# Performance work log

Hardware: AMD Instinct MI355X
Metric: run time of the kernel (lower is better)

The kernel has to match this reference:

```python
import jax, jax.numpy as jnp
import numpy as np

B, CH, H, W, D = 2, 32, 256, 512, 192


def setup_inputs() -> dict:
    key = jax.random.key(0)
    ks = jax.random.split(key, 10)
    def w(k, shape, fan_in):
        return jax.random.normal(k, shape, jnp.float32) * (1.0 / np.sqrt(fan_in))
    return {
        "x": jax.random.normal(ks[0], (B, CH, H, W), jnp.float32),
        "y": jax.random.normal(ks[1], (B, CH, H, W), jnp.float32),
        # encoder: 1x1 convs ch->64->32->1 (shared for x and y)
        "w1": w(ks[2], (64, CH), CH), "b1": w(ks[3], (64,), CH),
        "w2": w(ks[4], (32, 64), 64), "b2": w(ks[5], (32,), 64),
        "w3": w(ks[6], (1, 32), 32), "b3": w(ks[7], (1,), 32),
        # decoderl: 1x1 conv maxdisp->maxdisp (original code applies decoderl to BOTH volumes)
        "wd": w(ks[8], (D, D), D), "bd": w(ks[9], (D,), D),
    }


def _conv1x1(w, b, h):  # [O,C] x [B,C,H,W] -> [B,O,H,W]
    return jnp.einsum("oc,bchw->bohw", w, h) + b[None, :, None, None]


def _encoder(x, w1, b1, w2, b2, w3, b3):
    h = jax.nn.relu(x)
    h = jax.nn.relu(_conv1x1(w1, b1, h))
    h = jax.nn.relu(_conv1x1(w2, b2, h))
    h = jax.nn.relu(_conv1x1(w3, b3, h))
    return h[:, 0]  # squeeze channel -> [B,H,W]


def _cost_volumes(xf, yf):
    # costx[b,d,h,w] = xf[b,h,w+d] * yf[b,h,w]   (0 where w+d >= W)
    # costy[b,d,h,w] = xf[b,h,w]   * yf[b,h,w-d] (0 where w-d < 0)
    dgrid = jnp.arange(D)
    wgrid = jnp.arange(W)
    x_pad = jnp.pad(xf, ((0, 0), (0, 0), (0, D)))          # zero pad right
    xg = x_pad[:, :, wgrid[None, :] + dgrid[:, None]]       # [B,H,D,W]
    costx = (xg * yf[:, :, None, :]).transpose(0, 2, 1, 3)  # [B,D,H,W]
    y_pad = jnp.pad(yf, ((0, 0), (0, 0), (D, 0)))           # zero pad left
    yg = y_pad[:, :, wgrid[None, :] - dgrid[:, None] + D]   # [B,H,D,W]
    costy = (xf[:, :, None, :] * yg).transpose(0, 2, 1, 3)  # [B,D,H,W]
    return costx, costy


def reference(x, y, w1, b1, w2, b2, w3, b3, wd, bd):
    xf = _encoder(x, w1, b1, w2, b2, w3, b3)
    yf = _encoder(y, w1, b1, w2, b2, w3, b3)
    costx, costy = _cost_volumes(xf, yf)
    probx = jax.nn.softmax(_conv1x1(wd, bd, costx), axis=1)
    proby = jax.nn.softmax(_conv1x1(wd, bd, costy), axis=1)  # decoderl used for both, as in source
    disp_vals = jnp.arange(D, dtype=probx.dtype)
    dispx = jnp.einsum("bdhw,d->bhw", probx, disp_vals)
    dispy = jnp.einsum("bdhw,d->bhw", proby, disp_vals)
    return dispx, dispy
```

## Files before the change

kernel.cpp:

```cpp
#include <hip/hip_runtime.h>


typedef __attribute__((ext_vector_type(8)))  __bf16 bf16x8;
typedef __attribute__((ext_vector_type(4)))  float  f32x4;
typedef __attribute__((ext_vector_type(16))) float  f32x16;

#define MFMA32(a,b,c) __builtin_amdgcn_mfma_f32_32x32x16_bf16((a),(b),(c),0,0,0)
#define MFMA16(a,b,c) __builtin_amdgcn_mfma_f32_16x16x32_bf16((a),(b),(c),0,0,0)

constexpr int WW  = 512;
constexpr int HW  = 256 * 512;
constexpr int CHW = 32 * HW;
constexpr float LOG2E = 1.4426950408889634f;

constexpr size_t XFB_OFF = 0;
constexpr size_t WDP_OFF = 2 * 262144 * 2;
constexpr size_t BDP_OFF = WDP_OFF + 73728;

__global__ __launch_bounds__(512)
void panet_encode(const float* __restrict__ gx,  const float* __restrict__ gy,
                  const float* __restrict__ gw1, const float* __restrict__ gb1,
                  const float* __restrict__ gw2, const float* __restrict__ gb2,
                  const float* __restrict__ gw3, const float* __restrict__ gb3,
                  const float* __restrict__ gwd, const float* __restrict__ gbd,
                  char* __restrict__ ws)
{
  const int blk = blockIdx.x;
  const int tid = threadIdx.x;

  if (blk >= 1024) {
    const int pi = blk - 1024;
    unsigned short* wdp = (unsigned short*)(ws + WDP_OFF);
    for (int idx = tid; idx < 12 * 192; idx += 512) {
      const int oo = idx / 192;
      const int k  = idx - oo * 192;
      const int o  = 12 * pi + oo;
      const __bf16 v = (__bf16)gwd[o * 192 + k];
      wdp[o * 192 + k] = __builtin_bit_cast(unsigned short, v);
    }
    if (pi == 0) {
      float* bdp = (float*)(ws + BDP_OFF);
      if (tid < 192) bdp[tid] = gbd[tid] * LOG2E;
    }
    return;
  }

  const int t    = blk >> 9;
  const int bh   = blk & 511;
  const int lane = tid & 63;
  const int m    = lane & 15;
  const int g    = lane >> 4;
  const int wid  = tid >> 6;

  bf16x8 A1[4], A2[2][2];
  f32x4  bias1[4], bias2[2], w3v[2];
  #pragma unroll
  for (int Mt = 0; Mt < 4; ++Mt) {
    const float* p = gw1 + (16 * Mt + m) * 32 + 4 * g;
    const f32x4 u0 = *(const f32x4*)p;
    const f32x4 u1 = *(const f32x4*)(p + 16);
    #pragma unroll
    for (int j = 0; j < 4; ++j) { A1[Mt][j] = (__bf16)u0[j]; A1[Mt][j + 4] = (__bf16)u1[j]; }
    bias1[Mt] = *(const f32x4*)(gb1 + 16 * Mt + 4 * g);
  }
  #pragma unroll
  for (int Mt = 0; Mt < 2; ++Mt) {
    #pragma unroll
    for (int s = 0; s < 2; ++s) {
      const float* p = gw2 + (16 * Mt + m) * 64 + 32 * s + 4 * g;
      const f32x4 u0 = *(const f32x4*)p;
      const f32x4 u1 = *(const f32x4*)(p + 16);
      #pragma unroll
      for (int j = 0; j < 4; ++j) { A2[Mt][s][j] = (__bf16)u0[j]; A2[Mt][s][j + 4] = (__bf16)u1[j]; }
    }
    bias2[Mt] = *(const f32x4*)(gb2 + 16 * Mt + 4 * g);
    w3v[Mt]   = *(const f32x4*)(gw3 + 16 * Mt + 4 * g);
  }
  const float b3s = gb3[0];
  const f32x4 zf4 = {0.f, 0.f, 0.f, 0.f};
  const float* base = (t ? gy : gx) + (bh >> 8) * CHW + (bh & 255) * WW;
  unsigned short* xfb = (unsigned short*)(ws + XFB_OFF) + t * 262144 + bh * 512;

  for (int u = wid; u < 32; u += 8) {
    const int w0 = u << 4;
    const float* src = base + w0 + m;

    bf16x8 B1;
    #pragma unroll
    for (int j = 0; j < 8; ++j) {
      const int c = 16 * (j >> 2) + 4 * g + (j & 3);
      B1[j] = (__bf16)fmaxf(src[c * HW], 0.f);
    }
    f32x4 acc1[4];
    #pragma unroll
    for (int Mt = 0; Mt < 4; ++Mt) acc1[Mt] = MFMA16(A1[Mt], B1, zf4);

    bf16x8 B2[2];
    #pragma unroll
    for (int s = 0; s < 2; ++s) {
      #pragma unroll
      for (int j = 0; j < 4; ++j) {
        B2[s][j]     = (__bf16)fmaxf(acc1[2 * s][j]     + bias1[2 * s][j],     0.f);
        B2[s][j + 4] = (__bf16)fmaxf(acc1[2 * s + 1][j] + bias1[2 * s + 1][j], 0.f);
      }
    }
    f32x4 acc2[2];
    #pragma unroll
    for (int Mt = 0; Mt < 2; ++Mt)
      acc2[Mt] = MFMA16(A2[Mt][1], B2[1], MFMA16(A2[Mt][0], B2[0], zf4));

    float s3 = 0.f;
    #pragma unroll
    for (int Mt = 0; Mt < 2; ++Mt)
      #pragma unroll
      for (int r = 0; r < 4; ++r)
        s3 += w3v[Mt][r] * fmaxf(acc2[Mt][r] + bias2[Mt][r], 0.f);
    s3 += __shfl_xor(s3, 16);
    s3 += __shfl_xor(s3, 32);
    const float val = fmaxf(s3 + b3s, 0.f);

    if (lane < 16)
      xfb[w0 + m] = __builtin_bit_cast(unsigned short, (__bf16)val);
  }
}

constexpr int CPS    = 1424;
constexpr int K2_WD  = 0;
constexpr int K2_HK  = 25600;
constexpr int K2_BD  = K2_HK + 11392;
constexpr int K2_LDS = K2_BD + 768;

__global__ __launch_bounds__(512)
void panet_corr(const char* __restrict__ ws, float* __restrict__ gout)
{
  __shared__ __align__(16) char lds[K2_LDS];
  const int blk  = blockIdx.x;
  const int dir  = blk >> 9;
  const int bh   = blk & 511;
  const int tid  = threadIdx.x;
  const int lane = tid & 63;
  const int l31  = lane & 31;
  const int h    = lane >> 5;
  const int wid  = tid >> 6;

  const unsigned short* xfb = (const unsigned short*)(ws + XFB_OFF);
  const unsigned short* hs = xfb + (dir ? 262144 : 0) + bh * 512;
  const unsigned short* ss = xfb + (dir ? 0 : 262144) + bh * 512;

  {
    int* zp = (int*)(lds + K2_HK);
    for (int i = tid; i < 11392 / 4; i += 512) zp[i] = 0;
    const float* bdp = (const float*)(ws + BDP_OFF);
    if (tid < 192) ((float*)(lds + K2_BD))[tid] = bdp[tid];
  }
  __syncthreads();
  #pragma unroll
  for (int c = 0; c < 8; ++c) {
    const int e = tid;
    if (e + c <= 511)
      ((unsigned short*)(lds + K2_HK + c * CPS))[e] = hs[dir ? (511 - e - c) : (e + c)];
  }

  int bfb[2]; float sc[2];
  #pragma unroll
  for (int ct = 0; ct < 2; ++ct) {
    const int col = wid * 64 + ct * 32 + l31;
    const int I0  = dir ? (511 - col) : col;
    const int cc  = I0 & 7;
    bfb[ct] = K2_HK + cc * CPS + 2 * (I0 - cc) + 16 * h;
    sc[ct]  = LOG2E * __builtin_bit_cast(float, (unsigned)ss[col] << 16);
  }
  const int baseA = l31 * 400 + 16 * h;

  float stM[2] = {-3.4e38f, -3.4e38f};
  float stS[2] = {0.f, 0.f};
  float stW[2] = {0.f, 0.f};

  for (int stage = 0; stage < 3; ++stage) {
    if (stage) __syncthreads();
    for (int i = tid; i < 1536; i += 512) {
      const f32x4 v = *(const f32x4*)(ws + WDP_OFF + stage * 24576 + i * 16);
      const int row = i / 24;
      const int within = (i - row * 24) * 16;
      *(f32x4*)(lds + K2_WD + row * 400 + within) = v;
    }
    __syncthreads();

    f32x16 a00 = {0}, a01 = {0}, a10 = {0}, a11 = {0};
    #pragma unroll 2
    for (int ks = 0; ks < 12; ++ks) {
      const int ko = 32 * ks;
      const bf16x8 af0 = *(const bf16x8*)(lds + K2_WD + baseA + ko);
      const bf16x8 af1 = *(const bf16x8*)(lds + K2_WD + baseA + 12800 + ko);
      const bf16x8 bf0 = *(const bf16x8*)(lds + bfb[0] + ko);
      const bf16x8 bf1 = *(const bf16x8*)(lds + bfb[1] + ko);
      a00 = MFMA32(af0, bf0, a00);
      a01 = MFMA32(af0, bf1, a01);
      a10 = MFMA32(af1, bf0, a10);
      a11 = MFMA32(af1, bf1, a11);
    }

    #pragma unroll
    for (int ct = 0; ct < 2; ++ct) {
      const f32x16 A0 = ct ? a01 : a00;
      const f32x16 A1 = ct ? a11 : a10;
      float L[32];
      #pragma unroll
      for (int q = 0; q < 4; ++q) {
        const int rbase0 = 64 * stage + 8 * q + 4 * h;
        const f32x4 bd0 = *(const f32x4*)(lds + K2_BD + rbase0 * 4);
        const f32x4 bd1 = *(const f32x4*)(lds + K2_BD + (rbase0 + 32) * 4);
        #pragma unroll
        for (int r = 0; r < 4; ++r) {
          L[4 * q + r]      = fmaf(sc[ct], A0[4 * q + r], bd0[r]);
          L[16 + 4 * q + r] = fmaf(sc[ct], A1[4 * q + r], bd1[r]);
        }
      }
      float pm = L[0];
      #pragma unroll
      for (int i = 1; i < 32; ++i) pm = fmaxf(pm, L[i]);
      const float nm = fmaxf(stM[ct], pm);
      const float f  = exp2f(stM[ct] - nm);
      float ls = 0.f, lw = 0.f;
      #pragma unroll
      for (int i = 0; i < 32; ++i) {
        const float p = exp2f(L[i] - nm);
        const float o = (float)(64 * stage + ((i >> 4) << 5) + (i & 3) + (((i & 15) >> 2) << 3) + 4 * h);
        ls += p;
        lw = fmaf(o, p, lw);
      }
      stS[ct] = fmaf(stS[ct], f, ls);
      stW[ct] = fmaf(stW[ct], f, lw);
      stM[ct] = nm;
    }
  }

  float* outp = gout + dir * 262144 + bh * 512;
  #pragma unroll
  for (int ct = 0; ct < 2; ++ct) {
    const float Mo = __shfl_xor(stM[ct], 32);
    const float M  = fmaxf(stM[ct], Mo);
    const float f  = exp2f(stM[ct] - M);
    float sr = stS[ct] * f;
    float wr = stW[ct] * f;
    sr += __shfl_xor(sr, 32);
    wr += __shfl_xor(wr, 32);
    if (lane < 32) outp[wid * 64 + ct * 32 + l31] = wr / sr;
  }
}

extern "C" void kernel_launch(void* const* d_in, const int* in_sizes, int n_in,
                              void* d_out, int out_size, void* d_ws, size_t ws_size,
                              hipStream_t stream) {
  const float* x  = (const float*)d_in[0];
  const float* y  = (const float*)d_in[1];
  const float* w1 = (const float*)d_in[2];
  const float* b1 = (const float*)d_in[3];
  const float* w2 = (const float*)d_in[4];
  const float* b2 = (const float*)d_in[5];
  const float* w3 = (const float*)d_in[6];
  const float* b3 = (const float*)d_in[7];
  const float* wd = (const float*)d_in[8];
  const float* bd = (const float*)d_in[9];
  char* ws = (char*)d_ws;

  panet_encode<<<1040, 512, 0, stream>>>(x, y, w1, b1, w2, b2, w3, b3, wd, bd, ws);
  panet_corr<<<1024, 512, 0, stream>>>(ws, (float*)d_out);
}
```

Baseline: 89.24 us.

## Double-buffer decoder weight stages in LDS with register prefetch and tree reductions

The encode kernel now pre-pads the bf16 decoder weights into the 200-element row stride that the LDS layout uses, so each stage can be copied straight into LDS with contiguous 16-byte stores and no per-element index math. The corr kernel loads the next weight stage into registers before the MFMA loop, then writes it into a second LDS buffer after the softmax, which cuts the barriers per stage and overlaps global loads with compute. The online-softmax max is now a tree reduction and the sums use four partial accumulators with a folded offset term, which shortens the dependency chains. In exchange LDS use roughly doubles, which may lower occupancy, and register pressure rises from the prefetch buffers.

```diff
diff --git a/kernel.cpp b/kernel.cpp
--- a/kernel.cpp
+++ b/kernel.cpp
@@ -14,8 +14,9 @@
 constexpr float LOG2E = 1.4426950408889634f;
 
 constexpr size_t XFB_OFF = 0;
+constexpr int    STB     = 25600;
 constexpr size_t WDP_OFF = 2 * 262144 * 2;
-constexpr size_t BDP_OFF = WDP_OFF + 73728;
+constexpr size_t BDP_OFF = WDP_OFF + 3 * STB;
 
 __global__ __launch_bounds__(512)
 void panet_encode(const float* __restrict__ gx,  const float* __restrict__ gy,
@@ -31,12 +32,15 @@
   if (blk >= 1024) {
     const int pi = blk - 1024;
     unsigned short* wdp = (unsigned short*)(ws + WDP_OFF);
-    for (int idx = tid; idx < 12 * 192; idx += 512) {
-      const int oo = idx / 192;
-      const int k  = idx - oo * 192;
+    for (int idx = tid; idx < 12 * 200; idx += 512) {
+      const int oo = idx / 200;
+      const int k  = idx - oo * 200;
       const int o  = 12 * pi + oo;
-      const __bf16 v = (__bf16)gwd[o * 192 + k];
-      wdp[o * 192 + k] = __builtin_bit_cast(unsigned short, v);
+      const int stage = o >> 6;
+      const int r     = o & 63;
+      unsigned short v = 0;
+      if (k < 192) v = __builtin_bit_cast(unsigned short, (__bf16)gwd[o * 192 + k]);
+      wdp[stage * 12800 + r * 200 + k] = v;
     }
     if (pi == 0) {
       float* bdp = (float*)(ws + BDP_OFF);
@@ -126,7 +130,7 @@
 
 constexpr int CPS    = 1424;
 constexpr int K2_WD  = 0;
-constexpr int K2_HK  = 25600;
+constexpr int K2_HK  = 2 * STB;
 constexpr int K2_BD  = K2_HK + 11392;
 constexpr int K2_LDS = K2_BD + 768;
 
@@ -147,7 +151,14 @@
   const unsigned short* hs = xfb + (dir ? 262144 : 0) + bh * 512;
   const unsigned short* ss = xfb + (dir ? 0 : 262144) + bh * 512;
 
+  f32x4 streg[4];
+
   {
+    const char* src = ws + WDP_OFF;
+    #pragma unroll
+    for (int k = 0; k < 3; ++k) streg[k] = *(const f32x4*)(src + (tid + 512 * k) * 16);
+    if (tid < 64) streg[3] = *(const f32x4*)(src + (tid + 1536) * 16);
+
     int* zp = (int*)(lds + K2_HK);
     for (int i = tid; i < 11392 / 4; i += 512) zp[i] = 0;
     const float* bdp = (const float*)(ws + BDP_OFF);
@@ -160,6 +171,13 @@
     if (e + c <= 511)
       ((unsigned short*)(lds + K2_HK + c * CPS))[e] = hs[dir ? (511 - e - c) : (e + c)];
   }
+  {
+    char* dst = lds + K2_WD;
+    #pragma unroll
+    for (int k = 0; k < 3; ++k) *(f32x4*)(dst + (tid + 512 * k) * 16) = streg[k];
+    if (tid < 64) *(f32x4*)(dst + (tid + 1536) * 16) = streg[3];
+  }
+  __syncthreads();
 
   int bfb[2]; float sc[2];
   #pragma unroll
@@ -176,22 +194,21 @@
   float stS[2] = {0.f, 0.f};
   float stW[2] = {0.f, 0.f};
 
-  for (int stage = 0; stage < 3; ++stage) {
-    if (stage) __syncthreads();
-    for (int i = tid; i < 1536; i += 512) {
-      const f32x4 v = *(const f32x4*)(ws + WDP_OFF + stage * 24576 + i * 16);
-      const int row = i / 24;
-      const int within = (i - row * 24) * 16;
-      *(f32x4*)(lds + K2_WD + row * 400 + within) = v;
-    }
-    __syncthreads();
-
+  for (int s = 0; s < 3; ++s) {
+    if (s < 2) {
+      const char* src = ws + WDP_OFF + (s + 1) * STB;
+      #pragma unroll
+      for (int k = 0; k < 3; ++k) streg[k] = *(const f32x4*)(src + (tid + 512 * k) * 16);
+      if (tid < 64) streg[3] = *(const f32x4*)(src + (tid + 1536) * 16);
+    }
+
+    const int bufo = (s & 1) * STB;
     f32x16 a00 = {0}, a01 = {0}, a10 = {0}, a11 = {0};
     #pragma unroll 2
     for (int ks = 0; ks < 12; ++ks) {
       const int ko = 32 * ks;
-      const bf16x8 af0 = *(const bf16x8*)(lds + K2_WD + baseA + ko);
-      const bf16x8 af1 = *(const bf16x8*)(lds + K2_WD + baseA + 12800 + ko);
+      const bf16x8 af0 = *(const bf16x8*)(lds + K2_WD + bufo + baseA + ko);
+      const bf16x8 af1 = *(const bf16x8*)(lds + K2_WD + bufo + baseA + 12800 + ko);
       const bf16x8 bf0 = *(const bf16x8*)(lds + bfb[0] + ko);
       const bf16x8 bf1 = *(const bf16x8*)(lds + bfb[1] + ko);
       a00 = MFMA32(af0, bf0, a00);
@@ -204,34 +221,50 @@
     for (int ct = 0; ct < 2; ++ct) {
       const f32x16 A0 = ct ? a01 : a00;
       const f32x16 A1 = ct ? a11 : a10;
-      float L[32];
+      float L0[16], L1[16];
       #pragma unroll
       for (int q = 0; q < 4; ++q) {
-        const int rbase0 = 64 * stage + 8 * q + 4 * h;
-        const f32x4 bd0 = *(const f32x4*)(lds + K2_BD + rbase0 * 4);
-        const f32x4 bd1 = *(const f32x4*)(lds + K2_BD + (rbase0 + 32) * 4);
+        const f32x4 bd0 = *(const f32x4*)(lds + K2_BD + (64 * s + 8 * q + 4 * h) * 4);
+        const f32x4 bd1 = *(const f32x4*)(lds + K2_BD + (64 * s + 8 * q + 4 * h + 32) * 4);
         #pragma unroll
         for (int r = 0; r < 4; ++r) {
-          L[4 * q + r]      = fmaf(sc[ct], A0[4 * q + r], bd0[r]);
-          L[16 + 4 * q + r] = fmaf(sc[ct], A1[4 * q + r], bd1[r]);
+          L0[4 * q + r] = fmaf(sc[ct], A0[4 * q + r], bd0[r]);
+          L1[4 * q + r] = fmaf(sc[ct], A1[4 * q + r], bd1[r]);
         }
       }
-      float pm = L[0];
-      #pragma unroll
-      for (int i = 1; i < 32; ++i) pm = fmaxf(pm, L[i]);
-      const float nm = fmaxf(stM[ct], pm);
-      const float f  = exp2f(stM[ct] - nm);
-      float ls = 0.f, lw = 0.f;
-      #pragma unroll
-      for (int i = 0; i < 32; ++i) {
-        const float p = exp2f(L[i] - nm);
-        const float o = (float)(64 * stage + ((i >> 4) << 5) + (i & 3) + (((i & 15) >> 2) << 3) + 4 * h);
-        ls += p;
-        lw = fmaf(o, p, lw);
+      float t[16];
+      #pragma unroll
+      for (int i = 0; i < 16; ++i) t[i] = fmaxf(L0[i], L1[i]);
+      #pragma unroll
+      for (int off = 8; off > 0; off >>= 1)
+        #pragma unroll
+        for (int i = 0; i < off; ++i) t[i] = fmaxf(t[i], t[i + off]);
+      const float nm   = fmaxf(stM[ct], t[0]);
+      const float fold = exp2f(stM[ct] - nm);
+      float lsp[4] = {0.f, 0.f, 0.f, 0.f}, lwp[4] = {0.f, 0.f, 0.f, 0.f};
+      #pragma unroll
+      for (int i = 0; i < 16; ++i) {
+        const float c  = (float)((i & 3) + 8 * (i >> 2));
+        const float p0 = exp2f(L0[i] - nm);
+        const float p1 = exp2f(L1[i] - nm);
+        lsp[i & 3] += p0 + p1;
+        lwp[i & 3] = fmaf(c, p0, lwp[i & 3]);
+        lwp[i & 3] = fmaf(c + 32.f, p1, lwp[i & 3]);
       }
-      stS[ct] = fmaf(stS[ct], f, ls);
-      stW[ct] = fmaf(stW[ct], f, lw);
+      float ls = (lsp[0] + lsp[1]) + (lsp[2] + lsp[3]);
+      float lw = (lwp[0] + lwp[1]) + (lwp[2] + lwp[3]);
+      lw = fmaf((float)(64 * s + 4 * h), ls, lw);
+      stS[ct] = fmaf(stS[ct], fold, ls);
+      stW[ct] = fmaf(stW[ct], fold, lw);
       stM[ct] = nm;
+    }
+
+    if (s < 2) {
+      char* dst = lds + K2_WD + ((s + 1) & 1) * STB;
+      #pragma unroll
+      for (int k = 0; k < 3; ++k) *(f32x4*)(dst + (tid + 512 * k) * 16) = streg[k];
+      if (tid < 64) *(f32x4*)(dst + (tid + 1536) * 16) = streg[3];
+      __syncthreads();
     }
   }
 
```

Result: faster. 83.70 us (-6.2%).
